# Optimization experiments

Hardware: AMD Instinct MI355X
Metric: run time of the kernel (lower is better)

Reference implementation:

```python
import jax, jax.numpy as jnp
import numpy as np

GROUP = 32
HEADS = 8
EPS = 1e-5


def setup_inputs() -> dict:
    key = jax.random.key(0)
    k1, k2, k3 = jax.random.split(key, 3)
    C = 512
    x = jax.random.normal(k1, (8, C, 32, 32), dtype=jnp.float32)
    gn_w = jnp.ones((C,), dtype=jnp.float32)
    gn_b = jnp.zeros((C,), dtype=jnp.float32)
    # 1x1 convs == channel matmuls; init like torch conv default (kaiming-ish scale)
    w_qkv = jax.random.normal(k2, (3 * C, C), dtype=jnp.float32) * (1.0 / np.sqrt(C))
    w_proj = jax.random.normal(k3, (C, C), dtype=jnp.float32) * (1.0 / np.sqrt(C))
    return {"x": x, "gn_w": gn_w, "gn_b": gn_b, "w_qkv": w_qkv, "w_proj": w_proj}


def _forward(x, gn_w, gn_b, w_qkv, w_proj):
    B, C, H, W = x.shape
    N = H * W
    d = C // HEADS
    scale = d ** -0.5
    # GroupNorm over (channels_per_group, H, W)
    xg = x.reshape(B, GROUP, C // GROUP, H, W)
    mean = xg.mean(axis=(2, 3, 4), keepdims=True)
    var = xg.var(axis=(2, 3, 4), keepdims=True)
    xn = ((xg - mean) * jax.lax.rsqrt(var + EPS)).reshape(B, C, H, W)
    xn = xn * gn_w[None, :, None, None] + gn_b[None, :, None, None]
    # 1x1 conv QKV: [3C, C] x [B, C, H, W]
    qkv = jnp.einsum('oc,bchw->bohw', w_qkv, xn)
    q, k, v = jnp.split(qkv, 3, axis=1)

    def to_heads(t):  # b (h d) H W -> b h N d
        return t.reshape(B, HEADS, d, N).transpose(0, 1, 3, 2)

    q, k, v = to_heads(q), to_heads(k), to_heads(v)
    scores = jnp.einsum('bhid,bhjd->bhij', q, k) * scale
    probs = jax.nn.softmax(scores, axis=-1)
    out = jnp.einsum('bhij,bhjd->bhid', probs, v)
    # b h N d -> b (h d) H W
    out = out.transpose(0, 1, 3, 2).reshape(B, C, H, W)
    out = jnp.einsum('oc,bchw->bohw', w_proj, out)
    return x + out


def reference(x, gn_w, gn_b, w_qkv, w_proj):
    return _forward(x, gn_w, gn_b, w_qkv, w_proj)
```

## Files before the change

kernel.cpp:

```cpp
#include <hip/hip_runtime.h>

typedef __attribute__((ext_vector_type(4)))  float f32x4;
typedef __attribute__((ext_vector_type(16))) float f32x16;
typedef __attribute__((ext_vector_type(8)))  __bf16 bf16x8;
typedef __attribute__((ext_vector_type(8)))  unsigned short ushort8;

#define BATCH 8
#define CH    512
#define NN    1024
#define GRP   32
#define NHEAD 8
#define DH    64
#define QBLK  128
#define KBLK  64

static constexpr size_t OFF_STATS = 0;
static constexpr size_t OFF_WQB   = 4096;
static constexpr size_t OFF_WPB   = OFF_WQB + (size_t)1536*512*2;
static constexpr size_t OFF_XNT   = OFF_WPB + (size_t)512*512*2;
static constexpr size_t OFF_QKB   = OFF_XNT + (size_t)BATCH*NN*CH*2;
static constexpr size_t OFF_VT    = OFF_QKB + (size_t)BATCH*NN*1024*2;
static constexpr size_t OFF_ATTNT = OFF_VT  + (size_t)BATCH*CH*NN*2;

static __device__ __forceinline__ unsigned short f2bf(float f){
  union { float f; unsigned u; } cv; cv.f = f;
  unsigned u = cv.u;
  u += 0x7fffu + ((u >> 16) & 1u);
  return (unsigned short)(u >> 16);
}

static __device__ __forceinline__ unsigned pack2bf(float lo, float hi){
  union { __bf16 h[2]; unsigned u; } v;
  v.h[0] = (__bf16)lo; v.h[1] = (__bf16)hi;
  return v.u;
}

static __device__ __forceinline__ void plswap(unsigned &a, unsigned &b){
  asm("v_permlane32_swap_b32 %0, %1" : "+v"(a), "+v"(b));
}

static __device__ __forceinline__ void gload_lds16(const unsigned short* g, unsigned short* l){
  __builtin_amdgcn_global_load_lds((const __attribute__((address_space(1))) void*)g,
                                   (__attribute__((address_space(3))) void*)l, 16, 0, 0);
}

__global__ __launch_bounds__(256) void pre_k(const float* __restrict__ x,
                                             const float* __restrict__ wq, const float* __restrict__ wp,
                                             float* __restrict__ stats,
                                             unsigned short* __restrict__ wqb, unsigned short* __restrict__ wpb){
  int bid = blockIdx.x;
  if (bid < 256){
    int bg = bid;
    const float4* base = (const float4*)(x + (size_t)bg * (16*NN));
    float s = 0.f, ss = 0.f;
    #pragma unroll 4
    for (int idx = threadIdx.x; idx < 16*NN/4; idx += 256){
      float4 v = base[idx];
      s  += (v.x + v.y) + (v.z + v.w);
      ss += (v.x*v.x + v.y*v.y) + (v.z*v.z + v.w*v.w);
    }
    for (int off = 32; off > 0; off >>= 1){ s += __shfl_down(s, off); ss += __shfl_down(ss, off); }
    __shared__ float red[8];
    int w = threadIdx.x >> 6, l = threadIdx.x & 63;
    if (l == 0){ red[w*2] = s; red[w*2+1] = ss; }
    __syncthreads();
    if (threadIdx.x == 0){
      float S  = red[0]+red[2]+red[4]+red[6];
      float SS = red[1]+red[3]+red[5]+red[7];
      float mean = S * (1.f/(16*NN));
      float var  = SS * (1.f/(16*NN)) - mean*mean;
      stats[bg*2]   = mean;
      stats[bg*2+1] = rsqrtf(var + 1e-5f);
    }
  } else {
    int i = (bid - 256)*256 + threadIdx.x;
    if (i < 1536*512) wqb[i] = f2bf(wq[i]);
    if (i < 512*512)  wpb[i] = f2bf(wp[i]);
  }
}

__global__ __launch_bounds__(256) void gn_apply_k(const float* __restrict__ x, const float* __restrict__ stats,
                                                  const float* __restrict__ gw, const float* __restrict__ gb,
                                                  unsigned short* __restrict__ xnT){
  int b = blockIdx.z, c0 = blockIdx.y*64, n0 = blockIdx.x*64;
  __shared__ unsigned short T[64][65];
  int t = threadIdx.x;
  int nl = t & 63;
  int cb = t >> 6;
  #pragma unroll
  for (int r = 0; r < 16; ++r){
    int cl = cb + r*4;
    int c  = c0 + cl;
    float xv   = x[((size_t)b*CH + c)*NN + n0 + nl];
    float mean = stats[(b*GRP + (c>>4))*2];
    float rstd = stats[(b*GRP + (c>>4))*2 + 1];
    float sc   = rstd * gw[c];
    T[cl][nl]  = f2bf((xv - mean)*sc + gb[c]);
  }
  __syncthreads();
  #pragma unroll
  for (int r = 0; r < 16; ++r){
    int nlocal = cb + r*4;
    xnT[((size_t)b*NN + n0 + nlocal)*CH + c0 + nl] = T[nl][nlocal];
  }
}

__global__ __launch_bounds__(256) void qkv_gemm_k(const unsigned short* __restrict__ wq,
                                                  const unsigned short* __restrict__ xnT,
                                                  unsigned short* __restrict__ qkb,
                                                  unsigned short* __restrict__ vT){
  int b  = blockIdx.z;
  int m0 = blockIdx.y * 128;
  int n0 = blockIdx.x * 128;
  __shared__ unsigned short As[128][64];
  __shared__ unsigned short Bs[128][64];
  int t = threadIdx.x;
  int w = t >> 6, l = t & 63;
  int wm = w >> 1, wn = w & 1;
  f32x4 acc[4][4] = {};
  const unsigned short* Ag = wq  + (size_t)(m0 + w*32)*512;
  const unsigned short* Bg = xnT + ((size_t)b*NN + n0 + w*32)*512;
  int r8 = l >> 3;
  int c8 = ((l & 7) ^ r8) * 8;
  int lr = l & 15, lg = l >> 4;
  int xr = (lr & 7) << 3;
  for (int k0 = 0; k0 < 512; k0 += 64){
    #pragma unroll
    for (int i = 0; i < 4; ++i){
      gload_lds16(Ag + (size_t)(i*8 + r8)*512 + k0 + c8, &As[w*32 + i*8][0]);
      gload_lds16(Bg + (size_t)(i*8 + r8)*512 + k0 + c8, &Bs[w*32 + i*8][0]);
    }
    __syncthreads();
    #pragma unroll
    for (int ks = 0; ks < 2; ++ks){
      bf16x8 af[4], bfr[4];
      #pragma unroll
      for (int mf = 0; mf < 4; ++mf) af[mf]  = *(const bf16x8*)&As[wm*64 + mf*16 + lr][(ks*32 + lg*8) ^ xr];
      #pragma unroll
      for (int nf = 0; nf < 4; ++nf) bfr[nf] = *(const bf16x8*)&Bs[wn*64 + nf*16 + lr][(ks*32 + lg*8) ^ xr];
      #pragma unroll
      for (int mf = 0; mf < 4; ++mf)
        #pragma unroll
        for (int nf = 0; nf < 4; ++nf)
          acc[mf][nf] = __builtin_amdgcn_mfma_f32_16x16x32_bf16(af[mf], bfr[nf], acc[mf][nf], 0, 0, 0);
    }
    __syncthreads();
  }
  int lq = l >> 4;
  float scl = (m0 < 512) ? 0.18033688f : 1.0f;
  if (m0 < 1024){
    #pragma unroll
    for (int mf = 0; mf < 4; ++mf)
      #pragma unroll
      for (int nf = 0; nf < 4; ++nf)
        #pragma unroll
        for (int r = 0; r < 4; ++r){
          int o = m0 + wm*64 + mf*16 + lq*4 + r;
          int n = n0 + wn*64 + nf*16 + lr;
          qkb[((size_t)b*NN + n)*1024 + o] = f2bf(acc[mf][nf][r] * scl);
        }
  } else {
    #pragma unroll
    for (int mf = 0; mf < 4; ++mf)
      #pragma unroll
      for (int nf = 0; nf < 4; ++nf)
        #pragma unroll
        for (int r = 0; r < 4; ++r){
          int o = m0 + wm*64 + mf*16 + lq*4 + r;
          int n = n0 + wn*64 + nf*16 + lr;
          vT[((size_t)b*512 + (o - 1024))*NN + n] = f2bf(acc[mf][nf][r]);
        }
  }
}

#define STAGE_KV(TT, BUF)                                                                \
  {                                                                                      \
    int jj = (TT) * KBLK;                                                                \
    _Pragma("unroll") for (int ch = 0; ch < 2; ++ch){                                    \
      gload_lds16(Kg + (size_t)(jj + w*16 + ch*8 + srow)*1024 + scol,                    \
                  &KV[0][BUF][w*16 + ch*8][0]);                                          \
      gload_lds16(Vg + (size_t)(w*16 + ch*8 + srow)*NN + jj + scol,                      \
                  &KV[1][BUF][w*16 + ch*8][0]);                                          \
    }                                                                                    \
  }

__global__ __launch_bounds__(256) void attn_k(const unsigned short* __restrict__ qkb,
                                              const unsigned short* __restrict__ vT,
                                              unsigned short* __restrict__ attnT){
  int bh = blockIdx.x;
  int b = bh >> 3, h = bh & 7;
  int q0 = blockIdx.y * QBLK;
  int t = threadIdx.x;
  int w = t >> 6, l = t & 63;
  int lo5 = l & 31, hi = l >> 5;

  __shared__ unsigned short KV[2][2][64][64];

  int srow = l >> 3;
  int scol = ((l & 7) ^ srow) * 8;
  const unsigned short* Kg = qkb + (size_t)b*NN*1024 + 512 + h*DH;
  const unsigned short* Vg = vT  + (size_t)(b*NHEAD + h)*DH*NN;

  bf16x8 qf[4];
  #pragma unroll
  for (int ks = 0; ks < 4; ++ks)
    qf[ks] = *(const bf16x8*)(qkb + ((size_t)b*NN + q0 + w*32 + lo5)*1024 + h*DH + ks*16 + hi*8);

  float lsum = 0.f;
  f32x16 accO[2] = {};

  STAGE_KV(0, 0)
  __syncthreads();

  int xr = (lo5 & 7) * 8;

  for (int tt = 0; tt < 16; ++tt){
    int cur = tt & 1;
    if (tt < 15) STAGE_KV(tt + 1, cur ^ 1)

    bf16x8 kf[2][4];
    #pragma unroll
    for (int f = 0; f < 2; ++f)
      #pragma unroll
      for (int ks = 0; ks < 4; ++ks)
        kf[f][ks] = *(const bf16x8*)&KV[0][cur][f*32 + lo5][(ks*16 + hi*8) ^ xr];

    f32x16 sT0 = {}, sT1 = {};
    __builtin_amdgcn_s_setprio(1);
    #pragma unroll
    for (int ks = 0; ks < 4; ++ks)
      sT0 = __builtin_amdgcn_mfma_f32_32x32x16_bf16(kf[0][ks], qf[ks], sT0, 0, 0, 0);
    #pragma unroll
    for (int ks = 0; ks < 4; ++ks)
      sT1 = __builtin_amdgcn_mfma_f32_32x32x16_bf16(kf[1][ks], qf[ks], sT1, 0, 0, 0);
    __builtin_amdgcn_s_setprio(0);

    bf16x8 vf[2][4];
    #pragma unroll
    for (int c = 0; c < 2; ++c)
      #pragma unroll
      for (int m = 0; m < 4; ++m)
        vf[c][m] = *(const bf16x8*)&KV[1][cur][c*32 + lo5][(m*16 + hi*8) ^ xr];

    float p0[16], p1[16];
    #pragma unroll
    for (int r = 0; r < 16; ++r){
      p0[r] = exp2f(sT0[r]); lsum += p0[r];
      p1[r] = exp2f(sT1[r]); lsum += p1[r];
    }

    #pragma unroll
    for (int m = 0; m < 4; ++m){
      const float* pv = (m < 2) ? p0 : p1;
      int mm = (m & 1) * 8;
      unsigned x1 = pack2bf(pv[mm+0], pv[mm+1]);
      unsigned y1 = pack2bf(pv[mm+4], pv[mm+5]);
      unsigned x2 = pack2bf(pv[mm+2], pv[mm+3]);
      unsigned y2 = pack2bf(pv[mm+6], pv[mm+7]);
      plswap(x1, y1);
      plswap(x2, y2);
      union { unsigned u[4]; bf16x8 v; } pf;
      pf.u[0] = x1; pf.u[1] = x2; pf.u[2] = y1; pf.u[3] = y2;
      __builtin_amdgcn_s_setprio(1);
      accO[0] = __builtin_amdgcn_mfma_f32_32x32x16_bf16(pf.v, vf[0][m], accO[0], 0, 0, 0);
      accO[1] = __builtin_amdgcn_mfma_f32_32x32x16_bf16(pf.v, vf[1][m], accO[1], 0, 0, 0);
      __builtin_amdgcn_s_setprio(0);
    }
    __syncthreads();
  }

  lsum += __shfl_xor(lsum, 32);
  float inv = 1.f / lsum;

  float invq[16];
  #pragma unroll
  for (int r = 0; r < 16; ++r)
    invq[r] = __shfl(inv, (r & 3) + 8*(r >> 2) + 4*hi);

  #pragma unroll
  for (int r = 0; r < 16; ++r){
    int qr = (r & 3) + 8*(r >> 2) + 4*hi;
    unsigned short* dst = attnT + ((size_t)b*NN + q0 + w*32 + qr)*CH + h*DH + lo5;
    dst[0]  = f2bf(accO[0][r] * invq[r]);
    dst[32] = f2bf(accO[1][r] * invq[r]);
  }
}

__global__ __launch_bounds__(256) void proj_gemm_k(const unsigned short* __restrict__ wp,
                                                   const unsigned short* __restrict__ attnT,
                                                   const float* __restrict__ x, float* __restrict__ out){
  int b  = blockIdx.z;
  int m0 = blockIdx.y * 64;
  int n0 = blockIdx.x * 128;
  __shared__ unsigned short As[64][64];
  __shared__ unsigned short Bs[128][64];
  int t = threadIdx.x;
  int w = t >> 6, l = t & 63;
  int wm = w >> 1, wn = w & 1;
  f32x4 acc[2][4] = {};
  const unsigned short* Ag = wp    + (size_t)(m0 + w*16)*512;
  const unsigned short* Bg = attnT + ((size_t)b*NN + n0 + w*32)*512;
  int r8 = l >> 3;
  int c8 = ((l & 7) ^ r8) * 8;
  int lr = l & 15, lg = l >> 4;
  int xr = (lr & 7) << 3;
  for (int k0 = 0; k0 < 512; k0 += 64){
    #pragma unroll
    for (int i = 0; i < 2; ++i)
      gload_lds16(Ag + (size_t)(i*8 + r8)*512 + k0 + c8, &As[w*16 + i*8][0]);
    #pragma unroll
    for (int i = 0; i < 4; ++i)
      gload_lds16(Bg + (size_t)(i*8 + r8)*512 + k0 + c8, &Bs[w*32 + i*8][0]);
    __syncthreads();
    #pragma unroll
    for (int ks = 0; ks < 2; ++ks){
      bf16x8 af[2], bfr[4];
      #pragma unroll
      for (int mf = 0; mf < 2; ++mf) af[mf]  = *(const bf16x8*)&As[wm*32 + mf*16 + lr][(ks*32 + lg*8) ^ xr];
      #pragma unroll
      for (int nf = 0; nf < 4; ++nf) bfr[nf] = *(const bf16x8*)&Bs[wn*64 + nf*16 + lr][(ks*32 + lg*8) ^ xr];
      #pragma unroll
      for (int mf = 0; mf < 2; ++mf)
        #pragma unroll
        for (int nf = 0; nf < 4; ++nf)
          acc[mf][nf] = __builtin_amdgcn_mfma_f32_16x16x32_bf16(af[mf], bfr[nf], acc[mf][nf], 0, 0, 0);
    }
    __syncthreads();
  }
  int lq = l >> 4;
  #pragma unroll
  for (int mf = 0; mf < 2; ++mf)
    #pragma unroll
    for (int nf = 0; nf < 4; ++nf)
      #pragma unroll
      for (int r = 0; r < 4; ++r){
        int o = m0 + wm*32 + mf*16 + lq*4 + r;
        int n = n0 + wn*64 + nf*16 + lr;
        size_t idx = ((size_t)b*CH + o)*NN + n;
        out[idx] = x[idx] + acc[mf][nf][r];
      }
}

extern "C" void kernel_launch(void* const* d_in, const int* in_sizes, int n_in,
                              void* d_out, int out_size, void* d_ws, size_t ws_size,
                              hipStream_t stream){
  const float* x  = (const float*)d_in[0];
  const float* gw = (const float*)d_in[1];
  const float* gb = (const float*)d_in[2];
  const float* wq = (const float*)d_in[3];
  const float* wp = (const float*)d_in[4];
  float* out = (float*)d_out;
  char* ws = (char*)d_ws;
  float*          stats = (float*)(ws + OFF_STATS);
  unsigned short* wqb   = (unsigned short*)(ws + OFF_WQB);
  unsigned short* wpb   = (unsigned short*)(ws + OFF_WPB);
  unsigned short* xnT   = (unsigned short*)(ws + OFF_XNT);
  unsigned short* qkb   = (unsigned short*)(ws + OFF_QKB);
  unsigned short* vT    = (unsigned short*)(ws + OFF_VT);
  unsigned short* attnT = (unsigned short*)(ws + OFF_ATTNT);

  hipLaunchKernelGGL(pre_k,      dim3(3328),      dim3(256), 0, stream, x, wq, wp, stats, wqb, wpb);
  hipLaunchKernelGGL(gn_apply_k, dim3(16, 8, 8),  dim3(256), 0, stream, x, stats, gw, gb, xnT);
  hipLaunchKernelGGL(qkv_gemm_k, dim3(8, 12, 8),  dim3(256), 0, stream, wqb, xnT, qkb, vT);
  hipLaunchKernelGGL(attn_k,     dim3(64, 8),     dim3(256), 0, stream, qkb, vT, attnT);
  hipLaunchKernelGGL(proj_gemm_k,dim3(8, 8, 8),   dim3(256), 0, stream, wpb, attnT, x, out);
}
```

Baseline: 147.7 us.

## Split attention KV range across two wave groups and reduce partial outputs in LDS

The attention kernel now launches 512 threads per block. Two groups of four waves each process half of the 1024 keys for the same 128 queries, and their partial O accumulators and row sums are combined through shared memory at the end. This doubles the waves per block, which is meant to raise occupancy and latency hiding in a grid of only 512 blocks. The score and PV loops are also restructured per 32-key fragment to cut register pressure. In exchange it doubles LDS use per block and adds a final LDS reduction with an extra barrier.

```diff
diff --git a/kernel.cpp b/kernel.cpp
--- a/kernel.cpp
+++ b/kernel.cpp
@@ -175,114 +175,134 @@
 
 #define STAGE_KV(TT, BUF)                                                                \
   {                                                                                      \
-    int jj = (TT) * KBLK;                                                                \
+    int jj = kbase + (TT) * KBLK;                                                        \
     _Pragma("unroll") for (int ch = 0; ch < 2; ++ch){                                    \
-      gload_lds16(Kg + (size_t)(jj + w*16 + ch*8 + srow)*1024 + scol,                    \
-                  &KV[0][BUF][w*16 + ch*8][0]);                                          \
-      gload_lds16(Vg + (size_t)(w*16 + ch*8 + srow)*NN + jj + scol,                      \
-                  &KV[1][BUF][w*16 + ch*8][0]);                                          \
+      gload_lds16(Kg + (size_t)(jj + wl*16 + ch*8 + srow)*1024 + scol,                   \
+                  &KV[g][0][BUF][wl*16 + ch*8][0]);                                      \
+      gload_lds16(Vg + (size_t)(wl*16 + ch*8 + srow)*NN + jj + scol,                     \
+                  &KV[g][1][BUF][wl*16 + ch*8][0]);                                      \
     }                                                                                    \
   }
 
-__global__ __launch_bounds__(256) void attn_k(const unsigned short* __restrict__ qkb,
-                                              const unsigned short* __restrict__ vT,
-                                              unsigned short* __restrict__ attnT){
+__global__ __launch_bounds__(512, 4) void attn_k(const unsigned short* __restrict__ qkb,
+                                                 const unsigned short* __restrict__ vT,
+                                                 unsigned short* __restrict__ attnT){
   int bh = blockIdx.x;
   int b = bh >> 3, h = bh & 7;
   int q0 = blockIdx.y * QBLK;
   int t = threadIdx.x;
   int w = t >> 6, l = t & 63;
+  int wl = w & 3, g = w >> 2;
   int lo5 = l & 31, hi = l >> 5;
 
-  __shared__ unsigned short KV[2][2][64][64];
+  __shared__ unsigned short KV[2][2][2][64][64];
 
   int srow = l >> 3;
   int scol = ((l & 7) ^ srow) * 8;
   const unsigned short* Kg = qkb + (size_t)b*NN*1024 + 512 + h*DH;
   const unsigned short* Vg = vT  + (size_t)(b*NHEAD + h)*DH*NN;
+  int kbase = g * 512;
 
   bf16x8 qf[4];
   #pragma unroll
   for (int ks = 0; ks < 4; ++ks)
-    qf[ks] = *(const bf16x8*)(qkb + ((size_t)b*NN + q0 + w*32 + lo5)*1024 + h*DH + ks*16 + hi*8);
+    qf[ks] = *(const bf16x8*)(qkb + ((size_t)b*NN + q0 + wl*32 + lo5)*1024 + h*DH + ks*16 + hi*8);
 
   float lsum = 0.f;
-  f32x16 accO[2] = {};
+  f32x16 accO0 = {}, accO1 = {};
 
   STAGE_KV(0, 0)
   __syncthreads();
 
   int xr = (lo5 & 7) * 8;
 
-  for (int tt = 0; tt < 16; ++tt){
+  for (int tt = 0; tt < 8; ++tt){
     int cur = tt & 1;
-    if (tt < 15) STAGE_KV(tt + 1, cur ^ 1)
-
-    bf16x8 kf[2][4];
-    #pragma unroll
-    for (int f = 0; f < 2; ++f)
+    if (tt < 7) STAGE_KV(tt + 1, cur ^ 1)
+
+    #pragma unroll
+    for (int f = 0; f < 2; ++f){
+      bf16x8 kf[4];
       #pragma unroll
       for (int ks = 0; ks < 4; ++ks)
-        kf[f][ks] = *(const bf16x8*)&KV[0][cur][f*32 + lo5][(ks*16 + hi*8) ^ xr];
-
-    f32x16 sT0 = {}, sT1 = {};
-    __builtin_amdgcn_s_setprio(1);
-    #pragma unroll
-    for (int ks = 0; ks < 4; ++ks)
-      sT0 = __builtin_amdgcn_mfma_f32_32x32x16_bf16(kf[0][ks], qf[ks], sT0, 0, 0, 0);
-    #pragma unroll
-    for (int ks = 0; ks < 4; ++ks)
-      sT1 = __builtin_amdgcn_mfma_f32_32x32x16_bf16(kf[1][ks], qf[ks], sT1, 0, 0, 0);
-    __builtin_amdgcn_s_setprio(0);
-
-    bf16x8 vf[2][4];
-    #pragma unroll
-    for (int c = 0; c < 2; ++c)
-      #pragma unroll
-      for (int m = 0; m < 4; ++m)
-        vf[c][m] = *(const bf16x8*)&KV[1][cur][c*32 + lo5][(m*16 + hi*8) ^ xr];
-
-    float p0[16], p1[16];
+        kf[ks] = *(const bf16x8*)&KV[g][0][cur][f*32 + lo5][(ks*16 + hi*8) ^ xr];
+
+      f32x16 sT = {};
+      __builtin_amdgcn_s_setprio(1);
+      #pragma unroll
+      for (int ks = 0; ks < 4; ++ks)
+        sT = __builtin_amdgcn_mfma_f32_32x32x16_bf16(kf[ks], qf[ks], sT, 0, 0, 0);
+      __builtin_amdgcn_s_setprio(0);
+
+      float p[16];
+      #pragma unroll
+      for (int r = 0; r < 16; ++r){ p[r] = exp2f(sT[r]); lsum += p[r]; }
+
+      #pragma unroll
+      for (int mh = 0; mh < 2; ++mh){
+        int mc = ((f*2 + mh)*16 + hi*8) ^ xr;
+        bf16x8 vf0 = *(const bf16x8*)&KV[g][1][cur][lo5][mc];
+        bf16x8 vf1 = *(const bf16x8*)&KV[g][1][cur][32 + lo5][mc];
+        int mm = mh*8;
+        unsigned x1 = pack2bf(p[mm+0], p[mm+1]);
+        unsigned y1 = pack2bf(p[mm+4], p[mm+5]);
+        unsigned x2 = pack2bf(p[mm+2], p[mm+3]);
+        unsigned y2 = pack2bf(p[mm+6], p[mm+7]);
+        plswap(x1, y1);
+        plswap(x2, y2);
+        union { unsigned u[4]; bf16x8 v; } pf;
+        pf.u[0] = x1; pf.u[1] = x2; pf.u[2] = y1; pf.u[3] = y2;
+        __builtin_amdgcn_s_setprio(1);
+        accO0 = __builtin_amdgcn_mfma_f32_32x32x16_bf16(pf.v, vf0, accO0, 0, 0, 0);
+        accO1 = __builtin_amdgcn_mfma_f32_32x32x16_bf16(pf.v, vf1, accO1, 0, 0, 0);
+        __builtin_amdgcn_s_setprio(0);
+      }
+    }
+    __syncthreads();
+  }
+
+  float* Sc = (float*)&KV[0][0][0][0][0];
+  if (g == 1){
+    int base = wl*2048 + l*4;
+    #pragma unroll
+    for (int k = 0; k < 4; ++k){
+      f32x4 v0 = { accO0[k*4+0], accO0[k*4+1], accO0[k*4+2], accO0[k*4+3] };
+      *(f32x4*)&Sc[base + k*256] = v0;
+      f32x4 v1 = { accO1[k*4+0], accO1[k*4+1], accO1[k*4+2], accO1[k*4+3] };
+      *(f32x4*)&Sc[base + (4+k)*256] = v1;
+    }
+    Sc[8192 + wl*64 + l] = lsum;
+  }
+  __syncthreads();
+  if (g == 0){
+    int base = wl*2048 + l*4;
+    #pragma unroll
+    for (int k = 0; k < 4; ++k){
+      f32x4 v0 = *(const f32x4*)&Sc[base + k*256];
+      f32x4 v1 = *(const f32x4*)&Sc[base + (4+k)*256];
+      #pragma unroll
+      for (int j = 0; j < 4; ++j){
+        accO0[k*4+j] += v0[j];
+        accO1[k*4+j] += v1[j];
+      }
+    }
+    lsum += Sc[8192 + wl*64 + l];
+
+    lsum += __shfl_xor(lsum, 32);
+    float inv = 1.f / lsum;
+
+    float invq[16];
+    #pragma unroll
+    for (int r = 0; r < 16; ++r)
+      invq[r] = __shfl(inv, (r & 3) + 8*(r >> 2) + 4*hi);
+
     #pragma unroll
     for (int r = 0; r < 16; ++r){
-      p0[r] = exp2f(sT0[r]); lsum += p0[r];
-      p1[r] = exp2f(sT1[r]); lsum += p1[r];
-    }
-
-    #pragma unroll
-    for (int m = 0; m < 4; ++m){
-      const float* pv = (m < 2) ? p0 : p1;
-      int mm = (m & 1) * 8;
-      unsigned x1 = pack2bf(pv[mm+0], pv[mm+1]);
-      unsigned y1 = pack2bf(pv[mm+4], pv[mm+5]);
-      unsigned x2 = pack2bf(pv[mm+2], pv[mm+3]);
-      unsigned y2 = pack2bf(pv[mm+6], pv[mm+7]);
-      plswap(x1, y1);
-      plswap(x2, y2);
-      union { unsigned u[4]; bf16x8 v; } pf;
-      pf.u[0] = x1; pf.u[1] = x2; pf.u[2] = y1; pf.u[3] = y2;
-      __builtin_amdgcn_s_setprio(1);
-      accO[0] = __builtin_amdgcn_mfma_f32_32x32x16_bf16(pf.v, vf[0][m], accO[0], 0, 0, 0);
-      accO[1] = __builtin_amdgcn_mfma_f32_32x32x16_bf16(pf.v, vf[1][m], accO[1], 0, 0, 0);
-      __builtin_amdgcn_s_setprio(0);
-    }
-    __syncthreads();
-  }
-
-  lsum += __shfl_xor(lsum, 32);
-  float inv = 1.f / lsum;
-
-  float invq[16];
-  #pragma unroll
-  for (int r = 0; r < 16; ++r)
-    invq[r] = __shfl(inv, (r & 3) + 8*(r >> 2) + 4*hi);
-
-  #pragma unroll
-  for (int r = 0; r < 16; ++r){
-    int qr = (r & 3) + 8*(r >> 2) + 4*hi;
-    unsigned short* dst = attnT + ((size_t)b*NN + q0 + w*32 + qr)*CH + h*DH + lo5;
-    dst[0]  = f2bf(accO[0][r] * invq[r]);
-    dst[32] = f2bf(accO[1][r] * invq[r]);
+      int qr = (r & 3) + 8*(r >> 2) + 4*hi;
+      unsigned short* dst = attnT + ((size_t)b*NN + q0 + wl*32 + qr)*CH + h*DH + lo5;
+      dst[0]  = f2bf(accO0[r] * invq[r]);
+      dst[32] = f2bf(accO1[r] * invq[r]);
+    }
   }
 }
 
@@ -362,6 +382,6 @@
   hipLaunchKernelGGL(pre_k,      dim3(3328),      dim3(256), 0, stream, x, wq, wp, stats, wqb, wpb);
   hipLaunchKernelGGL(gn_apply_k, dim3(16, 8, 8),  dim3(256), 0, stream, x, stats, gw, gb, xnT);
   hipLaunchKernelGGL(qkv_gemm_k, dim3(8, 12, 8),  dim3(256), 0, stream, wqb, xnT, qkb, vT);
-  hipLaunchKernelGGL(attn_k,     dim3(64, 8),     dim3(256), 0, stream, qkb, vT, attnT);
+  hipLaunchKernelGGL(attn_k,     dim3(64, 8),     dim3(512), 0, stream, qkb, vT, attnT);
   hipLaunchKernelGGL(proj_gemm_k,dim3(8, 8, 8),   dim3(256), 0, stream, wpb, attnT, x, out);
 }
```

Result: faster. 141.3 us (-4.4%).
